# Optimization experiments

Measured on AMD Instinct MI355X. Metric: run time of the kernel, lower is better.

## Reference

```python
import jax, jax.numpy as jnp
import numpy as np

ALPHA = 16
M_FACTORS = [8, 16, 8]
N_FACTORS = [8, 16, 8]


def setup_inputs() -> dict:
    key = jax.random.key(0)
    ks = jax.random.split(key, 9)
    B, S, D = 8, 2048, 1024
    r = 8
    x = jax.random.normal(ks[0], (B, S, D), dtype=jnp.float32)
    W = jax.random.normal(ks[1], (D, D), dtype=jnp.float32) * 0.02
    b = jax.random.normal(ks[2], (D,), dtype=jnp.float32) * 0.02
    # m-cores: (r_prev, m_i, r_next), first rank = 1
    core0 = jax.random.normal(ks[3], (1, 8, r), dtype=jnp.float32) * 0.1
    core1 = jax.random.normal(ks[4], (r, 16, r), dtype=jnp.float32) * 0.1
    core2 = jax.random.normal(ks[5], (r, 8, r), dtype=jnp.float32) * 0.1
    # n-cores: (r_prev, n_i, r_next), last rank = 1
    core3 = jax.random.normal(ks[6], (r, 8, r), dtype=jnp.float32) * 0.1
    core4 = jax.random.normal(ks[7], (r, 16, r), dtype=jnp.float32) * 0.1
    core5 = jax.random.normal(ks[8], (r, 8, 1), dtype=jnp.float32) * 0.1
    return {"x": x, "W": W, "b": b, "core0": core0, "core1": core1,
            "core2": core2, "core3": core3, "core4": core4, "core5": core5}


def tensorized_multiplication(x, m_cores, n_cores, m_factors):
    B, S, _ = x.shape
    # [B, 1, S, m_k, ..., m_1] : input dim split into m_factors, reversed
    tt = x.reshape((B, S) + tuple(m_factors[::-1]))[:, None]
    for core in m_cores:
        # contract trailing m-factor and current rank, new rank at axis 1
        tt = jnp.einsum('br...m,rmp->bp...', tt, core)
    for core in n_cores:
        # expand n-factor at the end, carry rank at axis 1
        tt = jnp.einsum('br...,rnp->bp...n', tt, core)
    # tt: [B, 1, S, n_1, ..., n_k] -> [B, S, prod(n_factors)]
    return tt.reshape(B, S, -1)


def reference(x, W, b, core0, core1, core2, core3, core4, core5):
    z = tensorized_multiplication(x, [core0, core1, core2],
                                  [core3, core4, core5], M_FACTORS)
    base = jnp.einsum('bsd,od->bso', x, W) + b  # nn.Linear: x @ W.T + b
    return base + z * ALPHA
```

## Files before the change

### kernel.cpp

```cpp
#include <hip/hip_runtime.h>
#include <hip/hip_bf16.h>


#define D_DIM 1024
#define BS_ROWS 16384
#define ALPHA_F 16.0f
#define BM 128
#define BN 128
#define BK 32

using bf16   = __bf16;
using bf16x8 = __attribute__((ext_vector_type(8))) __bf16;
using bf16x4 = __attribute__((ext_vector_type(4))) __bf16;
using f32x4  = __attribute__((ext_vector_type(4))) float;

#define GPTR(p) (const __attribute__((address_space(1))) void*)(p)
#define SPTR(p) (__attribute__((address_space(3))) void*)(p)

__global__ __launch_bounds__(256) void build_weff_fused_kernel(
    const float* __restrict__ W,
    const float* __restrict__ c0, const float* __restrict__ c1,
    const float* __restrict__ c2, const float* __restrict__ c3,
    const float* __restrict__ c4, const float* __restrict__ c5,
    bf16* __restrict__ Weff)
{
    __shared__ float t2[1024];
    __shared__ float Msh[8192];
    const int tid = threadIdx.x;
    const int o = blockIdx.x;

    for (int e = tid; e < 1024; e += 256) {
        int p2 = e & 7, i2i1 = e >> 3;
        int i1 = i2i1 & 7, i2 = i2i1 >> 3;
        float s = 0.f;
        for (int p1 = 0; p1 < 8; ++p1)
            s += c0[i1 * 8 + p1] * c1[p1 * 128 + i2 * 8 + p2];
        t2[e] = s;
    }
    __syncthreads();
    for (int e = tid; e < 8192; e += 256) {
        int p3 = e & 7, d = e >> 3;
        int i1 = d & 7, i2 = (d >> 3) & 15, i3 = d >> 7;
        float s = 0.f;
        for (int p2 = 0; p2 < 8; ++p2)
            s += t2[(i2 * 8 + i1) * 8 + p2] * c2[p2 * 64 + i3 * 8 + p3];
        Msh[e] = s;
    }

    int n1 = o >> 7, nn = o & 127, n2 = nn >> 3, n3 = nn & 7;
    float v[8];
    for (int p4 = 0; p4 < 8; ++p4) {
        float s = 0.f;
        for (int p5 = 0; p5 < 8; ++p5)
            s += c4[p4 * 128 + n2 * 8 + p5] * c5[p5 * 8 + n3];
        v[p4] = s;
    }
    float ncol[8];
    for (int r3 = 0; r3 < 8; ++r3) {
        float s = 0.f;
        for (int p4 = 0; p4 < 8; ++p4)
            s += c3[r3 * 64 + n1 * 8 + p4] * v[p4];
        ncol[r3] = s;
    }
    __syncthreads();

    int d0 = tid * 4;
    f32x4 w = *(const f32x4*)&W[o * D_DIM + d0];
    bf16x4 res;
    for (int k = 0; k < 4; ++k) {
        float acc = 0.f;
        for (int r = 0; r < 8; ++r)
            acc += Msh[(d0 + k) * 8 + r] * ncol[r];
        res[k] = (bf16)(w[k] + ALPHA_F * acc);
    }
    *(bf16x4*)&Weff[o * D_DIM + d0] = res;
}

__global__ void cast_x_kernel(const float* __restrict__ X, bf16* __restrict__ Xb)
{
    int i = (blockIdx.x * 256 + threadIdx.x) * 8;
    f32x4 a = *(const f32x4*)&X[i];
    f32x4 b = *(const f32x4*)&X[i + 4];
    bf16x8 v;
    v[0] = (bf16)a[0]; v[1] = (bf16)a[1]; v[2] = (bf16)a[2]; v[3] = (bf16)a[3];
    v[4] = (bf16)b[0]; v[5] = (bf16)b[1]; v[6] = (bf16)b[2]; v[7] = (bf16)b[3];
    *(bf16x8*)&Xb[i] = v;
}

__global__ __launch_bounds__(256) void gemm_bb_kernel(
    const bf16* __restrict__ Xb,
    const bf16* __restrict__ Weff,
    const float* __restrict__ bias,
    float* __restrict__ Out)
{
    __shared__ __align__(16) bf16 As[BM][BK];
    __shared__ __align__(16) bf16 Bs[BN][BK];

    const int tid  = threadIdx.x;
    const int wave = tid >> 6, lane = tid & 63;
    const int mtile = blockIdx.x, ntile = blockIdx.y;
    const int wr = wave >> 1, wc = wave & 1;
    const int l15 = lane & 15, quad = lane >> 4;

    const int srow = wave * 32 + (lane >> 2);
    const int skof = (((lane & 3) ^ ((lane >> 3) & 3)) * 8);
    const bf16* asrc0 = Xb  + (size_t)(mtile * BM + srow) * D_DIM + skof;
    const bf16* asrc1 = asrc0 + 16 * D_DIM;
    const bf16* bsrc0 = Weff + (size_t)(ntile * BN + srow) * D_DIM + skof;
    const bf16* bsrc1 = bsrc0 + 16 * D_DIM;
    char* abase = (char*)&As[0][0];
    char* bbase = (char*)&Bs[0][0];
    void* adst0 = abase + wave * 2048;
    void* adst1 = abase + wave * 2048 + 1024;
    void* bdst0 = bbase + wave * 2048;
    void* bdst1 = bbase + wave * 2048 + 1024;

    const int fchunk = (quad ^ ((l15 >> 1) & 3)) * 8;

    f32x4 acc[4][4];
    for (int i = 0; i < 4; ++i)
        for (int j = 0; j < 4; ++j)
            for (int r = 0; r < 4; ++r) acc[i][j][r] = 0.f;

    for (int kt = 0; kt < D_DIM / BK; ++kt) {
        const int ko = kt * BK;
        __builtin_amdgcn_global_load_lds(GPTR(asrc0 + ko), SPTR(adst0), 16, 0, 0);
        __builtin_amdgcn_global_load_lds(GPTR(asrc1 + ko), SPTR(adst1), 16, 0, 0);
        __builtin_amdgcn_global_load_lds(GPTR(bsrc0 + ko), SPTR(bdst0), 16, 0, 0);
        __builtin_amdgcn_global_load_lds(GPTR(bsrc1 + ko), SPTR(bdst1), 16, 0, 0);

        __syncthreads();

        bf16x8 af[4], bfr[4];
        for (int i = 0; i < 4; ++i)
            af[i] = *(const bf16x8*)&As[wr * 64 + i * 16 + l15][fchunk];
        for (int j = 0; j < 4; ++j)
            bfr[j] = *(const bf16x8*)&Bs[wc * 64 + j * 16 + l15][fchunk];
        for (int i = 0; i < 4; ++i)
            for (int j = 0; j < 4; ++j)
                acc[i][j] = __builtin_amdgcn_mfma_f32_16x16x32_bf16(
                    af[i], bfr[j], acc[i][j], 0, 0, 0);

        __syncthreads();
    }

    float bj[4];
    for (int j = 0; j < 4; ++j)
        bj[j] = bias[ntile * BN + wc * 64 + j * 16 + l15];
    for (int i = 0; i < 4; ++i) {
        int row0 = mtile * BM + wr * 64 + i * 16 + quad * 4;
        for (int r = 0; r < 4; ++r) {
            float* orow = Out + (size_t)(row0 + r) * D_DIM + ntile * BN + wc * 64 + l15;
            for (int j = 0; j < 4; ++j)
                orow[j * 16] = acc[i][j][r] + bj[j];
        }
    }
}

__global__ __launch_bounds__(256) void gemm_bias_kernel(
    const float* __restrict__ X,
    const bf16* __restrict__ Weff,
    const float* __restrict__ bias,
    float* __restrict__ Out)
{
    __shared__ __align__(16) bf16 As[BM][BK];
    __shared__ __align__(16) bf16 Bs[BN][BK];

    const int tid  = threadIdx.x;
    const int wave = tid >> 6, lane = tid & 63;
    const int mtile = blockIdx.x, ntile = blockIdx.y;
    const int wr = wave >> 1, wc = wave & 1;
    const int l15 = lane & 15, quad = lane >> 4;

    const int ar = tid >> 1, ah = tid & 1;
    const float* xsrc = X + (size_t)(mtile * BM + ar) * D_DIM + ah * 16;
    bf16* adst = &As[ar][ah * 16];

    const bf16* bsrc0 = Weff + (size_t)(ntile * BN + wave * 32 + (lane >> 2)) * D_DIM
                        + (lane & 3) * 8;
    const bf16* bsrc1 = bsrc0 + 16 * D_DIM;
    char* bbase = (char*)&Bs[0][0];
    void* bdst0 = bbase + wave * 2048;
    void* bdst1 = bbase + wave * 2048 + 1024;

    f32x4 acc[4][4];
    for (int i = 0; i < 4; ++i)
        for (int j = 0; j < 4; ++j)
            for (int r = 0; r < 4; ++r) acc[i][j][r] = 0.f;

    for (int kt = 0; kt < D_DIM / BK; ++kt) {
        __builtin_amdgcn_global_load_lds(GPTR(bsrc0 + kt * BK), SPTR(bdst0), 16, 0, 0);
        __builtin_amdgcn_global_load_lds(GPTR(bsrc1 + kt * BK), SPTR(bdst1), 16, 0, 0);

        const f32x4* xp = (const f32x4*)(xsrc + kt * BK);
        f32x4 f0 = xp[0], f1 = xp[1], f2 = xp[2], f3 = xp[3];
        bf16x8 p0, p1;
        p0[0] = (bf16)f0[0]; p0[1] = (bf16)f0[1]; p0[2] = (bf16)f0[2]; p0[3] = (bf16)f0[3];
        p0[4] = (bf16)f1[0]; p0[5] = (bf16)f1[1]; p0[6] = (bf16)f1[2]; p0[7] = (bf16)f1[3];
        p1[0] = (bf16)f2[0]; p1[1] = (bf16)f2[1]; p1[2] = (bf16)f2[2]; p1[3] = (bf16)f2[3];
        p1[4] = (bf16)f3[0]; p1[5] = (bf16)f3[1]; p1[6] = (bf16)f3[2]; p1[7] = (bf16)f3[3];
        *(bf16x8*)adst = p0;
        *(bf16x8*)(adst + 8) = p1;

        __syncthreads();

        bf16x8 af[4], bfr[4];
        for (int i = 0; i < 4; ++i)
            af[i] = *(const bf16x8*)&As[wr * 64 + i * 16 + l15][quad * 8];
        for (int j = 0; j < 4; ++j)
            bfr[j] = *(const bf16x8*)&Bs[wc * 64 + j * 16 + l15][quad * 8];
        for (int i = 0; i < 4; ++i)
            for (int j = 0; j < 4; ++j)
                acc[i][j] = __builtin_amdgcn_mfma_f32_16x16x32_bf16(
                    af[i], bfr[j], acc[i][j], 0, 0, 0);

        __syncthreads();
    }

    float bj[4];
    for (int j = 0; j < 4; ++j)
        bj[j] = bias[ntile * BN + wc * 64 + j * 16 + l15];
    for (int i = 0; i < 4; ++i) {
        int row0 = mtile * BM + wr * 64 + i * 16 + quad * 4;
        for (int r = 0; r < 4; ++r) {
            float* orow = Out + (size_t)(row0 + r) * D_DIM + ntile * BN + wc * 64 + l15;
            for (int j = 0; j < 4; ++j)
                orow[j * 16] = acc[i][j][r] + bj[j];
        }
    }
}

extern "C" void kernel_launch(void* const* d_in, const int* in_sizes, int n_in,
                              void* d_out, int out_size, void* d_ws, size_t ws_size,
                              hipStream_t stream) {
    const float* x  = (const float*)d_in[0];
    const float* W  = (const float*)d_in[1];
    const float* b  = (const float*)d_in[2];
    const float* c0 = (const float*)d_in[3];
    const float* c1 = (const float*)d_in[4];
    const float* c2 = (const float*)d_in[5];
    const float* c3 = (const float*)d_in[6];
    const float* c4 = (const float*)d_in[7];
    const float* c5 = (const float*)d_in[8];
    float* out = (float*)d_out;

    char* ws = (char*)d_ws;
    bf16* Weff = (bf16*)ws;
    bf16* Xb   = (bf16*)(ws + 4u * 1024u * 1024u);
    const size_t need = 4u * 1024u * 1024u + (size_t)BS_ROWS * D_DIM * 2u;

    build_weff_fused_kernel<<<D_DIM, 256, 0, stream>>>(W, c0, c1, c2, c3, c4, c5, Weff);

    dim3 grid(BS_ROWS / BM, D_DIM / BN);
    if (ws_size >= need) {
        cast_x_kernel<<<(BS_ROWS * D_DIM) / (256 * 8), 256, 0, stream>>>(x, Xb);
        gemm_bb_kernel<<<grid, 256, 0, stream>>>(Xb, Weff, b, out);
    } else {
        gemm_bias_kernel<<<grid, 256, 0, stream>>>(x, Weff, b, out);
    }
}
```

Measured before the change: 191.7 us.

## Merge Weff build with X cast and double GEMM K-tile to 64

```diff
diff --git a/kernel.cpp b/kernel.cpp
--- a/kernel.cpp
+++ b/kernel.cpp
@@ -7,7 +7,6 @@
 #define ALPHA_F 16.0f
 #define BM 128
 #define BN 128
-#define BK 32
 
 using bf16   = __bf16;
 using bf16x8 = __attribute__((ext_vector_type(8))) __bf16;
@@ -16,6 +15,220 @@
 
 #define GPTR(p) (const __attribute__((address_space(1))) void*)(p)
 #define SPTR(p) (__attribute__((address_space(3))) void*)(p)
+
+__global__ __launch_bounds__(256) void prep_kernel(
+    const float* __restrict__ X,
+    const float* __restrict__ W,
+    const float* __restrict__ c0, const float* __restrict__ c1,
+    const float* __restrict__ c2, const float* __restrict__ c3,
+    const float* __restrict__ c4, const float* __restrict__ c5,
+    bf16* __restrict__ Weff, bf16* __restrict__ Xb)
+{
+    __shared__ float t2[1024];
+    __shared__ float Msh[8192];
+    const int tid = threadIdx.x;
+
+    if (blockIdx.x >= 1024) {
+        size_t i = ((size_t)(blockIdx.x - 1024) * 256 + tid) * 8;
+        f32x4 a = *(const f32x4*)&X[i];
+        f32x4 b = *(const f32x4*)&X[i + 4];
+        bf16x8 v;
+        v[0] = (bf16)a[0]; v[1] = (bf16)a[1]; v[2] = (bf16)a[2]; v[3] = (bf16)a[3];
+        v[4] = (bf16)b[0]; v[5] = (bf16)b[1]; v[6] = (bf16)b[2]; v[7] = (bf16)b[3];
+        *(bf16x8*)&Xb[i] = v;
+        return;
+    }
+
+    const int o = blockIdx.x;
+    for (int e = tid; e < 1024; e += 256) {
+        int p2 = e & 7, i2i1 = e >> 3;
+        int i1 = i2i1 & 7, i2 = i2i1 >> 3;
+        float s = 0.f;
+        for (int p1 = 0; p1 < 8; ++p1)
+            s += c0[i1 * 8 + p1] * c1[p1 * 128 + i2 * 8 + p2];
+        t2[e] = s;
+    }
+    __syncthreads();
+    for (int e = tid; e < 8192; e += 256) {
+        int p3 = e & 7, d = e >> 3;
+        int i1 = d & 7, i2 = (d >> 3) & 15, i3 = d >> 7;
+        float s = 0.f;
+        for (int p2 = 0; p2 < 8; ++p2)
+            s += t2[(i2 * 8 + i1) * 8 + p2] * c2[p2 * 64 + i3 * 8 + p3];
+        Msh[e] = s;
+    }
+
+    int n1 = o >> 7, nn = o & 127, n2 = nn >> 3, n3 = nn & 7;
+    float v[8];
+    for (int p4 = 0; p4 < 8; ++p4) {
+        float s = 0.f;
+        for (int p5 = 0; p5 < 8; ++p5)
+            s += c4[p4 * 128 + n2 * 8 + p5] * c5[p5 * 8 + n3];
+        v[p4] = s;
+    }
+    float ncol[8];
+    for (int r3 = 0; r3 < 8; ++r3) {
+        float s = 0.f;
+        for (int p4 = 0; p4 < 8; ++p4)
+            s += c3[r3 * 64 + n1 * 8 + p4] * v[p4];
+        ncol[r3] = s;
+    }
+    __syncthreads();
+
+    int d0 = tid * 4;
+    f32x4 w = *(const f32x4*)&W[o * D_DIM + d0];
+    bf16x4 res;
+    for (int k = 0; k < 4; ++k) {
+        float acc = 0.f;
+        for (int r = 0; r < 8; ++r)
+            acc += Msh[(d0 + k) * 8 + r] * ncol[r];
+        res[k] = (bf16)(w[k] + ALPHA_F * acc);
+    }
+    *(bf16x4*)&Weff[o * D_DIM + d0] = res;
+}
+
+__global__ __launch_bounds__(256) void gemm_bb_kernel(
+    const bf16* __restrict__ Xb,
+    const bf16* __restrict__ Weff,
+    const float* __restrict__ bias,
+    float* __restrict__ Out)
+{
+    __shared__ __align__(16) bf16 As[BM][64];
+    __shared__ __align__(16) bf16 Bs[BN][64];
+
+    const int tid  = threadIdx.x;
+    const int wave = tid >> 6, lane = tid & 63;
+    const int mtile = blockIdx.x, ntile = blockIdx.y;
+    const int wr = wave >> 1, wc = wave & 1;
+    const int l15 = lane & 15, quad = lane >> 4;
+
+    const int srow = wave * 32 + (lane >> 3);
+    const int gchunk = (lane & 7) ^ (lane >> 3);
+    const bf16* asrc = Xb   + (size_t)(mtile * BM + srow) * D_DIM + gchunk * 8;
+    const bf16* bsrc = Weff + (size_t)(ntile * BN + srow) * D_DIM + gchunk * 8;
+    char* abase = (char*)&As[0][0] + wave * 4096;
+    char* bbase = (char*)&Bs[0][0] + wave * 4096;
+
+    const int rsw = l15 & 7;
+
+    f32x4 acc[4][4];
+    for (int i = 0; i < 4; ++i)
+        for (int j = 0; j < 4; ++j)
+            for (int r = 0; r < 4; ++r) acc[i][j][r] = 0.f;
+
+    for (int kt = 0; kt < D_DIM / 64; ++kt) {
+        const int ko = kt * 64;
+        for (int j = 0; j < 4; ++j) {
+            __builtin_amdgcn_global_load_lds(GPTR(asrc + (size_t)j * 8 * D_DIM + ko),
+                                             SPTR(abase + j * 1024), 16, 0, 0);
+            __builtin_amdgcn_global_load_lds(GPTR(bsrc + (size_t)j * 8 * D_DIM + ko),
+                                             SPTR(bbase + j * 1024), 16, 0, 0);
+        }
+
+        __syncthreads();
+
+        for (int kk = 0; kk < 2; ++kk) {
+            const int lc = kk * 4 + quad;
+            const int sc = (lc ^ rsw) * 8;
+            bf16x8 af[4], bfr[4];
+            for (int i = 0; i < 4; ++i)
+                af[i] = *(const bf16x8*)&As[wr * 64 + i * 16 + l15][sc];
+            for (int j = 0; j < 4; ++j)
+                bfr[j] = *(const bf16x8*)&Bs[wc * 64 + j * 16 + l15][sc];
+            for (int i = 0; i < 4; ++i)
+                for (int j = 0; j < 4; ++j)
+                    acc[i][j] = __builtin_amdgcn_mfma_f32_16x16x32_bf16(
+                        af[i], bfr[j], acc[i][j], 0, 0, 0);
+        }
+
+        __syncthreads();
+    }
+
+    float bj[4];
+    for (int j = 0; j < 4; ++j)
+        bj[j] = bias[ntile * BN + wc * 64 + j * 16 + l15];
+    for (int i = 0; i < 4; ++i) {
+        int row0 = mtile * BM + wr * 64 + i * 16 + quad * 4;
+        for (int r = 0; r < 4; ++r) {
+            float* orow = Out + (size_t)(row0 + r) * D_DIM + ntile * BN + wc * 64 + l15;
+            for (int j = 0; j < 4; ++j)
+                orow[j * 16] = acc[i][j][r] + bj[j];
+        }
+    }
+}
+
+__global__ __launch_bounds__(256) void gemm_bias_kernel(
+    const float* __restrict__ X,
+    const bf16* __restrict__ Weff,
+    const float* __restrict__ bias,
+    float* __restrict__ Out)
+{
+    __shared__ __align__(16) bf16 As[BM][32];
+    __shared__ __align__(16) bf16 Bs[BN][32];
+
+    const int tid  = threadIdx.x;
+    const int wave = tid >> 6, lane = tid & 63;
+    const int mtile = blockIdx.x, ntile = blockIdx.y;
+    const int wr = wave >> 1, wc = wave & 1;
+    const int l15 = lane & 15, quad = lane >> 4;
+
+    const int ar = tid >> 1, ah = tid & 1;
+    const float* xsrc = X + (size_t)(mtile * BM + ar) * D_DIM + ah * 16;
+    bf16* adst = &As[ar][ah * 16];
+
+    const bf16* bsrc0 = Weff + (size_t)(ntile * BN + wave * 32 + (lane >> 2)) * D_DIM
+                        + (lane & 3) * 8;
+    const bf16* bsrc1 = bsrc0 + 16 * D_DIM;
+    char* bbase = (char*)&Bs[0][0];
+    void* bdst0 = bbase + wave * 2048;
+    void* bdst1 = bbase + wave * 2048 + 1024;
+
+    f32x4 acc[4][4];
+    for (int i = 0; i < 4; ++i)
+        for (int j = 0; j < 4; ++j)
+            for (int r = 0; r < 4; ++r) acc[i][j][r] = 0.f;
+
+    for (int kt = 0; kt < D_DIM / 32; ++kt) {
+        __builtin_amdgcn_global_load_lds(GPTR(bsrc0 + kt * 32), SPTR(bdst0), 16, 0, 0);
+        __builtin_amdgcn_global_load_lds(GPTR(bsrc1 + kt * 32), SPTR(bdst1), 16, 0, 0);
+
+        const f32x4* xp = (const f32x4*)(xsrc + kt * 32);
+        f32x4 f0 = xp[0], f1 = xp[1], f2 = xp[2], f3 = xp[3];
+        bf16x8 p0, p1;
+        p0[0] = (bf16)f0[0]; p0[1] = (bf16)f0[1]; p0[2] = (bf16)f0[2]; p0[3] = (bf16)f0[3];
+        p0[4] = (bf16)f1[0]; p0[5] = (bf16)f1[1]; p0[6] = (bf16)f1[2]; p0[7] = (bf16)f1[3];
+        p1[0] = (bf16)f2[0]; p1[1] = (bf16)f2[1]; p1[2] = (bf16)f2[2]; p1[3] = (bf16)f2[3];
+        p1[4] = (bf16)f3[0]; p1[5] = (bf16)f3[1]; p1[6] = (bf16)f3[2]; p1[7] = (bf16)f3[3];
+        *(bf16x8*)adst = p0;
+        *(bf16x8*)(adst + 8) = p1;
+
+        __syncthreads();
+
+        bf16x8 af[4], bfr[4];
+        for (int i = 0; i < 4; ++i)
+            af[i] = *(const bf16x8*)&As[wr * 64 + i * 16 + l15][quad * 8];
+        for (int j = 0; j < 4; ++j)
+            bfr[j] = *(const bf16x8*)&Bs[wc * 64 + j * 16 + l15][quad * 8];
+        for (int i = 0; i < 4; ++i)
+            for (int j = 0; j < 4; ++j)
+                acc[i][j] = __builtin_amdgcn_mfma_f32_16x16x32_bf16(
+                    af[i], bfr[j], acc[i][j], 0, 0, 0);
+
+        __syncthreads();
+    }
+
+    float bj[4];
+    for (int j = 0; j < 4; ++j)
+        bj[j] = bias[ntile * BN + wc * 64 + j * 16 + l15];
+    for (int i = 0; i < 4; ++i) {
+        int row0 = mtile * BM + wr * 64 + i * 16 + quad * 4;
+        for (int r = 0; r < 4; ++r) {
+            float* orow = Out + (size_t)(row0 + r) * D_DIM + ntile * BN + wc * 64 + l15;
+            for (int j = 0; j < 4; ++j)
+                orow[j * 16] = acc[i][j][r] + bj[j];
+        }
+    }
+}
 
 __global__ __launch_bounds__(256) void build_weff_fused_kernel(
     const float* __restrict__ W,
@@ -46,7 +259,6 @@
             s += t2[(i2 * 8 + i1) * 8 + p2] * c2[p2 * 64 + i3 * 8 + p3];
         Msh[e] = s;
     }
-
     int n1 = o >> 7, nn = o & 127, n2 = nn >> 3, n3 = nn & 7;
     float v[8];
     for (int p4 = 0; p4 < 8; ++p4) {
@@ -74,160 +286,6 @@
         res[k] = (bf16)(w[k] + ALPHA_F * acc);
     }
     *(bf16x4*)&Weff[o * D_DIM + d0] = res;
-}
-
-__global__ void cast_x_kernel(const float* __restrict__ X, bf16* __restrict__ Xb)
-{
-    int i = (blockIdx.x * 256 + threadIdx.x) * 8;
-    f32x4 a = *(const f32x4*)&X[i];
-    f32x4 b = *(const f32x4*)&X[i + 4];
-    bf16x8 v;
-    v[0] = (bf16)a[0]; v[1] = (bf16)a[1]; v[2] = (bf16)a[2]; v[3] = (bf16)a[3];
-    v[4] = (bf16)b[0]; v[5] = (bf16)b[1]; v[6] = (bf16)b[2]; v[7] = (bf16)b[3];
-    *(bf16x8*)&Xb[i] = v;
-}
-
-__global__ __launch_bounds__(256) void gemm_bb_kernel(
-    const bf16* __restrict__ Xb,
-    const bf16* __restrict__ Weff,
-    const float* __restrict__ bias,
-    float* __restrict__ Out)
-{
-    __shared__ __align__(16) bf16 As[BM][BK];
-    __shared__ __align__(16) bf16 Bs[BN][BK];
-
-    const int tid  = threadIdx.x;
-    const int wave = tid >> 6, lane = tid & 63;
-    const int mtile = blockIdx.x, ntile = blockIdx.y;
-    const int wr = wave >> 1, wc = wave & 1;
-    const int l15 = lane & 15, quad = lane >> 4;
-
-    const int srow = wave * 32 + (lane >> 2);
-    const int skof = (((lane & 3) ^ ((lane >> 3) & 3)) * 8);
-    const bf16* asrc0 = Xb  + (size_t)(mtile * BM + srow) * D_DIM + skof;
-    const bf16* asrc1 = asrc0 + 16 * D_DIM;
-    const bf16* bsrc0 = Weff + (size_t)(ntile * BN + srow) * D_DIM + skof;
-    const bf16* bsrc1 = bsrc0 + 16 * D_DIM;
-    char* abase = (char*)&As[0][0];
-    char* bbase = (char*)&Bs[0][0];
-    void* adst0 = abase + wave * 2048;
-    void* adst1 = abase + wave * 2048 + 1024;
-    void* bdst0 = bbase + wave * 2048;
-    void* bdst1 = bbase + wave * 2048 + 1024;
-
-    const int fchunk = (quad ^ ((l15 >> 1) & 3)) * 8;
-
-    f32x4 acc[4][4];
-    for (int i = 0; i < 4; ++i)
-        for (int j = 0; j < 4; ++j)
-            for (int r = 0; r < 4; ++r) acc[i][j][r] = 0.f;
-
-    for (int kt = 0; kt < D_DIM / BK; ++kt) {
-        const int ko = kt * BK;
-        __builtin_amdgcn_global_load_lds(GPTR(asrc0 + ko), SPTR(adst0), 16, 0, 0);
-        __builtin_amdgcn_global_load_lds(GPTR(asrc1 + ko), SPTR(adst1), 16, 0, 0);
-        __builtin_amdgcn_global_load_lds(GPTR(bsrc0 + ko), SPTR(bdst0), 16, 0, 0);
-        __builtin_amdgcn_global_load_lds(GPTR(bsrc1 + ko), SPTR(bdst1), 16, 0, 0);
-
-        __syncthreads();
-
-        bf16x8 af[4], bfr[4];
-        for (int i = 0; i < 4; ++i)
-            af[i] = *(const bf16x8*)&As[wr * 64 + i * 16 + l15][fchunk];
-        for (int j = 0; j < 4; ++j)
-            bfr[j] = *(const bf16x8*)&Bs[wc * 64 + j * 16 + l15][fchunk];
-        for (int i = 0; i < 4; ++i)
-            for (int j = 0; j < 4; ++j)
-                acc[i][j] = __builtin_amdgcn_mfma_f32_16x16x32_bf16(
-                    af[i], bfr[j], acc[i][j], 0, 0, 0);
-
-        __syncthreads();
-    }
-
-    float bj[4];
-    for (int j = 0; j < 4; ++j)
-        bj[j] = bias[ntile * BN + wc * 64 + j * 16 + l15];
-    for (int i = 0; i < 4; ++i) {
-        int row0 = mtile * BM + wr * 64 + i * 16 + quad * 4;
-        for (int r = 0; r < 4; ++r) {
-            float* orow = Out + (size_t)(row0 + r) * D_DIM + ntile * BN + wc * 64 + l15;
-            for (int j = 0; j < 4; ++j)
-                orow[j * 16] = acc[i][j][r] + bj[j];
-        }
-    }
-}
-
-__global__ __launch_bounds__(256) void gemm_bias_kernel(
-    const float* __restrict__ X,
-    const bf16* __restrict__ Weff,
-    const float* __restrict__ bias,
-    float* __restrict__ Out)
-{
-    __shared__ __align__(16) bf16 As[BM][BK];
-    __shared__ __align__(16) bf16 Bs[BN][BK];
-
-    const int tid  = threadIdx.x;
-    const int wave = tid >> 6, lane = tid & 63;
-    const int mtile = blockIdx.x, ntile = blockIdx.y;
-    const int wr = wave >> 1, wc = wave & 1;
-    const int l15 = lane & 15, quad = lane >> 4;
-
-    const int ar = tid >> 1, ah = tid & 1;
-    const float* xsrc = X + (size_t)(mtile * BM + ar) * D_DIM + ah * 16;
-    bf16* adst = &As[ar][ah * 16];
-
-    const bf16* bsrc0 = Weff + (size_t)(ntile * BN + wave * 32 + (lane >> 2)) * D_DIM
-                        + (lane & 3) * 8;
-    const bf16* bsrc1 = bsrc0 + 16 * D_DIM;
-    char* bbase = (char*)&Bs[0][0];
-    void* bdst0 = bbase + wave * 2048;
-    void* bdst1 = bbase + wave * 2048 + 1024;
-
-    f32x4 acc[4][4];
-    for (int i = 0; i < 4; ++i)
-        for (int j = 0; j < 4; ++j)
-            for (int r = 0; r < 4; ++r) acc[i][j][r] = 0.f;
-
-    for (int kt = 0; kt < D_DIM / BK; ++kt) {
-        __builtin_amdgcn_global_load_lds(GPTR(bsrc0 + kt * BK), SPTR(bdst0), 16, 0, 0);
-        __builtin_amdgcn_global_load_lds(GPTR(bsrc1 + kt * BK), SPTR(bdst1), 16, 0, 0);
-
-        const f32x4* xp = (const f32x4*)(xsrc + kt * BK);
-        f32x4 f0 = xp[0], f1 = xp[1], f2 = xp[2], f3 = xp[3];
-        bf16x8 p0, p1;
-        p0[0] = (bf16)f0[0]; p0[1] = (bf16)f0[1]; p0[2] = (bf16)f0[2]; p0[3] = (bf16)f0[3];
-        p0[4] = (bf16)f1[0]; p0[5] = (bf16)f1[1]; p0[6] = (bf16)f1[2]; p0[7] = (bf16)f1[3];
-        p1[0] = (bf16)f2[0]; p1[1] = (bf16)f2[1]; p1[2] = (bf16)f2[2]; p1[3] = (bf16)f2[3];
-        p1[4] = (bf16)f3[0]; p1[5] = (bf16)f3[1]; p1[6] = (bf16)f3[2]; p1[7] = (bf16)f3[3];
-        *(bf16x8*)adst = p0;
-        *(bf16x8*)(adst + 8) = p1;
-
-        __syncthreads();
-
-        bf16x8 af[4], bfr[4];
-        for (int i = 0; i < 4; ++i)
-            af[i] = *(const bf16x8*)&As[wr * 64 + i * 16 + l15][quad * 8];
-        for (int j = 0; j < 4; ++j)
-            bfr[j] = *(const bf16x8*)&Bs[wc * 64 + j * 16 + l15][quad * 8];
-        for (int i = 0; i < 4; ++i)
-            for (int j = 0; j < 4; ++j)
-                acc[i][j] = __builtin_amdgcn_mfma_f32_16x16x32_bf16(
-                    af[i], bfr[j], acc[i][j], 0, 0, 0);
-
-        __syncthreads();
-    }
-
-    float bj[4];
-    for (int j = 0; j < 4; ++j)
-        bj[j] = bias[ntile * BN + wc * 64 + j * 16 + l15];
-    for (int i = 0; i < 4; ++i) {
-        int row0 = mtile * BM + wr * 64 + i * 16 + quad * 4;
-        for (int r = 0; r < 4; ++r) {
-            float* orow = Out + (size_t)(row0 + r) * D_DIM + ntile * BN + wc * 64 + l15;
-            for (int j = 0; j < 4; ++j)
-                orow[j * 16] = acc[i][j][r] + bj[j];
-        }
-    }
 }
 
 extern "C" void kernel_launch(void* const* d_in, const int* in_sizes, int n_in,
@@ -249,13 +307,13 @@
     bf16* Xb   = (bf16*)(ws + 4u * 1024u * 1024u);
     const size_t need = 4u * 1024u * 1024u + (size_t)BS_ROWS * D_DIM * 2u;
 
-    build_weff_fused_kernel<<<D_DIM, 256, 0, stream>>>(W, c0, c1, c2, c3, c4, c5, Weff);
-
     dim3 grid(BS_ROWS / BM, D_DIM / BN);
     if (ws_size >= need) {
-        cast_x_kernel<<<(BS_ROWS * D_DIM) / (256 * 8), 256, 0, stream>>>(x, Xb);
+        prep_kernel<<<1024 + 8192, 256, 0, stream>>>(x, W, c0, c1, c2, c3, c4, c5,
+                                                     Weff, Xb);
         gemm_bb_kernel<<<grid, 256, 0, stream>>>(Xb, Weff, b, out);
     } else {
+        build_weff_fused_kernel<<<D_DIM, 256, 0, stream>>>(W, c0, c1, c2, c3, c4, c5, Weff);
         gemm_bias_kernel<<<grid, 256, 0, stream>>>(x, Weff, b, out);
     }
 }
```

Measured after the change: 182.2 us. -4.9%, faster.
